# Optimization experiments

Hardware: AMD Instinct MI355X
Metric: run time of the kernel (lower is better)

Reference implementation:

```python
import jax, jax.numpy as jnp
import numpy as np

NEG_INF = -1.0e9
VALID_THRESH = -1.0e8
EPS = 1e-12


def _l2_normalize(x):
    n = jnp.linalg.norm(x, axis=-1, keepdims=True)
    return x / jnp.maximum(n, EPS)


def setup_inputs() -> dict:
    key = jax.random.key(0)
    k1, k2, k3, k4 = jax.random.split(key, 4)
    B, Nq, Nd, D = 64, 32, 256, 128
    return {
        "query_embeds": jax.random.normal(k1, (B, Nq, D), dtype=jnp.float32),
        "query_mask": jax.random.randint(k2, (B, Nq), 0, 2, dtype=jnp.int32),
        "doc_embeds": jax.random.normal(k3, (B, Nd, D), dtype=jnp.float32),
        "doc_mask": jax.random.randint(k4, (B, Nd), 0, 2, dtype=jnp.int32),
    }


def reference(query_embeds, query_mask, doc_embeds, doc_mask):
    # normalize=True, symmetric=True path
    q = _l2_normalize(query_embeds)
    d = _l2_normalize(doc_embeds)
    qm = query_mask.astype(jnp.float32)[..., None]  # [B, Nq, 1]
    dm = doc_mask.astype(jnp.float32)[..., None]    # [B, Nd, 1]
    q = q * qm
    d = d * dm

    # token_sims: [Bq, Bd, Nq, Nd]
    token_sims = jnp.einsum("qtd,csd->qcts", q, d)
    # pair mask: [Bq,1,Nq,1] * [1,Bd,1,Nd]
    mask = qm[:, None, :, :] * dm[None, :, :, 0][:, :, None, :].transpose(1, 0, 2, 3)
    masked_sims = jnp.where(mask > 0, token_sims, NEG_INF)

    # query -> doc max over doc tokens
    q2d = jnp.max(masked_sims, axis=-1)          # [Bq, Bd, Nq]
    valid_q = (q2d > VALID_THRESH).astype(jnp.float32)
    q2d = jnp.where(valid_q > 0, q2d, 0.0)
    cnt_q = jnp.maximum(jnp.sum(valid_q, axis=-1), 1.0)
    q2d_score = jnp.sum(q2d, axis=-1) / cnt_q    # [Bq, Bd]

    # doc -> query max over query tokens
    d2q = jnp.max(masked_sims, axis=-2)          # [Bq, Bd, Nd]
    valid_d = (d2q > VALID_THRESH).astype(jnp.float32)
    d2q = jnp.where(valid_d > 0, d2q, 0.0)
    cnt_d = jnp.maximum(jnp.sum(valid_d, axis=-1), 1.0)
    d2q_score = jnp.sum(d2q, axis=-1) / cnt_d    # [Bq, Bd]

    return (q2d_score + d2q_score) / 2.0
```

## Files before the change

### kernel.cpp

```cpp
#include <hip/hip_runtime.h>
#include <hip/hip_bf16.h>

typedef short bf16x8 __attribute__((ext_vector_type(8)));
typedef float f32x4 __attribute__((ext_vector_type(4)));

#define B_   64
#define NQ   32
#define ND   256
#define DIM  128
#define NEG_INF_F (-1.0e9f)
#define VALID_F   (-1.0e8f)

__global__ __launch_bounds__(256) void normalize_rows(
    const float* __restrict__ q, const int* __restrict__ qmask,
    const float* __restrict__ d, const int* __restrict__ dmask,
    __hip_bfloat16* __restrict__ qn, __hip_bfloat16* __restrict__ dn)
{
    const int l   = threadIdx.x & 63;
    const int row = blockIdx.x * 4 + (threadIdx.x >> 6);

    const float* src;
    __hip_bfloat16* dst;
    int m;
    if (row < B_ * NQ) {
        src = q + row * DIM;  dst = qn + row * DIM;  m = qmask[row];
    } else {
        const int r2 = row - B_ * NQ;
        src = d + r2 * DIM;   dst = dn + r2 * DIM;   m = dmask[r2];
    }

    const float2 v = *reinterpret_cast<const float2*>(src + l * 2);
    float ss = v.x * v.x + v.y * v.y;
    #pragma unroll
    for (int off = 1; off <= 32; off <<= 1) ss += __shfl_xor(ss, off);

    const float scale = m ? (1.0f / fmaxf(sqrtf(ss), 1e-12f)) : 0.0f;

    __hip_bfloat162 o;
    o.x = __float2bfloat16(v.x * scale);
    o.y = __float2bfloat16(v.y * scale);
    *reinterpret_cast<__hip_bfloat162*>(dst + l * 2) = o;
}

__global__ __launch_bounds__(256) void chamfer_main(
    const __hip_bfloat16* __restrict__ qn,
    const __hip_bfloat16* __restrict__ dn,
    const int* __restrict__ qmask,
    const int* __restrict__ dmask,
    float* __restrict__ out)
{
    const int bq = blockIdx.x >> 6;
    const int bd = blockIdx.x & 63;
    const int tid = threadIdx.x;
    const int w  = tid >> 6;
    const int l  = tid & 63;
    const int lr = l & 15;
    const int lk = l >> 4;

    const __hip_bfloat16* Q  = qn + bq * (NQ * DIM);
    const __hip_bfloat16* Dp = dn + (bd * ND + w * 64) * DIM;

    f32x4 acc[2][4] = {};

    #pragma unroll
    for (int kk = 0; kk < 4; ++kk) {
        const int k0 = kk * 32 + lk * 8;
        const bf16x8 a0 = *reinterpret_cast<const bf16x8*>(Q + lr * DIM + k0);
        const bf16x8 a1 = *reinterpret_cast<const bf16x8*>(Q + (16 + lr) * DIM + k0);
        bf16x8 bfr[4];
        #pragma unroll
        for (int ni = 0; ni < 4; ++ni)
            bfr[ni] = *reinterpret_cast<const bf16x8*>(Dp + (ni * 16 + lr) * DIM + k0);
        #pragma unroll
        for (int ni = 0; ni < 4; ++ni) {
            acc[0][ni] = __builtin_amdgcn_mfma_f32_16x16x32_bf16(a0, bfr[ni], acc[0][ni], 0, 0, 0);
            acc[1][ni] = __builtin_amdgcn_mfma_f32_16x16x32_bf16(a1, bfr[ni], acc[1][ni], 0, 0, 0);
        }
    }

    int qmv[2][4];
    #pragma unroll
    for (int mi = 0; mi < 2; ++mi)
        #pragma unroll
        for (int r = 0; r < 4; ++r)
            qmv[mi][r] = qmask[bq * NQ + mi * 16 + lk * 4 + r];
    int dmv[4];
    #pragma unroll
    for (int ni = 0; ni < 4; ++ni)
        dmv[ni] = dmask[bq * ND + w * 64 + ni * 16 + lr];

    float rmax[2][4];
    float cmax[4];
    #pragma unroll
    for (int ni = 0; ni < 4; ++ni) cmax[ni] = NEG_INF_F;
    #pragma unroll
    for (int mi = 0; mi < 2; ++mi) {
        #pragma unroll
        for (int r = 0; r < 4; ++r) {
            float rm = NEG_INF_F;
            #pragma unroll
            for (int ni = 0; ni < 4; ++ni) {
                const float v = (qmv[mi][r] && dmv[ni]) ? acc[mi][ni][r] : NEG_INF_F;
                rm = fmaxf(rm, v);
                cmax[ni] = fmaxf(cmax[ni], v);
            }
            rmax[mi][r] = rm;
        }
    }

    #pragma unroll
    for (int ni = 0; ni < 4; ++ni) {
        cmax[ni] = fmaxf(cmax[ni], __shfl_xor(cmax[ni], 16));
        cmax[ni] = fmaxf(cmax[ni], __shfl_xor(cmax[ni], 32));
    }
    float sd = 0.0f, cd = 0.0f;
    if (lk == 0) {
        #pragma unroll
        for (int ni = 0; ni < 4; ++ni)
            if (cmax[ni] > VALID_F) { sd += cmax[ni]; cd += 1.0f; }
    }
    #pragma unroll
    for (int off = 1; off <= 32; off <<= 1) {
        sd += __shfl_xor(sd, off);
        cd += __shfl_xor(cd, off);
    }

    __shared__ float s_rmax[4][NQ];
    __shared__ float s_sd[4], s_cd[4];
    if (l == 0) { s_sd[w] = sd; s_cd[w] = cd; }

    #pragma unroll
    for (int mi = 0; mi < 2; ++mi) {
        #pragma unroll
        for (int r = 0; r < 4; ++r) {
            #pragma unroll
            for (int off = 1; off <= 8; off <<= 1)
                rmax[mi][r] = fmaxf(rmax[mi][r], __shfl_xor(rmax[mi][r], off));
        }
    }
    if (lr == 0) {
        #pragma unroll
        for (int mi = 0; mi < 2; ++mi)
            #pragma unroll
            for (int r = 0; r < 4; ++r)
                s_rmax[w][mi * 16 + lk * 4 + r] = rmax[mi][r];
    }
    __syncthreads();

    if (w == 0) {
        float v = NEG_INF_F;
        if (l < NQ) {
            #pragma unroll
            for (int wv = 0; wv < 4; ++wv) v = fmaxf(v, s_rmax[wv][l]);
        }
        float sq = 0.0f, cq = 0.0f;
        if (l < NQ && v > VALID_F) { sq = v; cq = 1.0f; }
        #pragma unroll
        for (int off = 1; off <= 32; off <<= 1) {
            sq += __shfl_xor(sq, off);
            cq += __shfl_xor(cq, off);
        }
        if (l == 0) {
            const float q2d = sq / fmaxf(cq, 1.0f);
            const float sdt = s_sd[0] + s_sd[1] + s_sd[2] + s_sd[3];
            const float cdt = s_cd[0] + s_cd[1] + s_cd[2] + s_cd[3];
            const float d2q = sdt / fmaxf(cdt, 1.0f);
            out[bq * B_ + bd] = 0.5f * (q2d + d2q);
        }
    }
}

extern "C" void kernel_launch(void* const* d_in, const int* in_sizes, int n_in,
                              void* d_out, int out_size, void* d_ws, size_t ws_size,
                              hipStream_t stream) {
    const float* q  = (const float*)d_in[0];
    const int*   qm = (const int*)d_in[1];
    const float* d  = (const float*)d_in[2];
    const int*   dm = (const int*)d_in[3];
    float* out = (float*)d_out;

    __hip_bfloat16* qn = (__hip_bfloat16*)d_ws;
    __hip_bfloat16* dn = qn + (B_ * NQ) * DIM;

    normalize_rows<<<(B_ * NQ + B_ * ND) / 4, 256, 0, stream>>>(q, qm, d, dm, qn, dn);
    chamfer_main<<<B_ * B_, 256, 0, stream>>>(qn, dn, qm, dm, out);
}
```

Measured before the change: 117.2 us.

## Tile four query batches per block to reuse doc fragments, vectorize normalize

Each chamfer block now processes four query batches against one document tile, loading the document bf16 fragments once and reusing them across all four MFMA groups. The grid shrinks by four and each wave finalizes one query batch's score. The normalize kernel is also widened so each thread handles eight elements with 16-byte loads and stores. The exchange is higher accumulator register pressure and less block-level parallelism.

New measurement: 115.5 us. About the same (-1.4%).

```diff
diff --git a/kernel.cpp b/kernel.cpp
--- a/kernel.cpp
+++ b/kernel.cpp
@@ -2,12 +2,14 @@
 #include <hip/hip_bf16.h>
 
 typedef short bf16x8 __attribute__((ext_vector_type(8)));
+typedef short short8 __attribute__((ext_vector_type(8)));
 typedef float f32x4 __attribute__((ext_vector_type(4)));
 
 #define B_   64
 #define NQ   32
 #define ND   256
 #define DIM  128
+#define MT   4
 #define NEG_INF_F (-1.0e9f)
 #define VALID_F   (-1.0e8f)
 
@@ -16,8 +18,9 @@
     const float* __restrict__ d, const int* __restrict__ dmask,
     __hip_bfloat16* __restrict__ qn, __hip_bfloat16* __restrict__ dn)
 {
-    const int l   = threadIdx.x & 63;
-    const int row = blockIdx.x * 4 + (threadIdx.x >> 6);
+    const int tid  = threadIdx.x;
+    const int sub  = tid & 15;
+    const int row  = blockIdx.x * 16 + (tid >> 4);
 
     const float* src;
     __hip_bfloat16* dst;
@@ -29,17 +32,23 @@
         src = d + r2 * DIM;   dst = dn + r2 * DIM;   m = dmask[r2];
     }
 
-    const float2 v = *reinterpret_cast<const float2*>(src + l * 2);
-    float ss = v.x * v.x + v.y * v.y;
-    #pragma unroll
-    for (int off = 1; off <= 32; off <<= 1) ss += __shfl_xor(ss, off);
+    const float4 v0 = *reinterpret_cast<const float4*>(src + sub * 8);
+    const float4 v1 = *reinterpret_cast<const float4*>(src + sub * 8 + 4);
+    float ss = v0.x*v0.x + v0.y*v0.y + v0.z*v0.z + v0.w*v0.w
+             + v1.x*v1.x + v1.y*v1.y + v1.z*v1.z + v1.w*v1.w;
+    #pragma unroll
+    for (int off = 1; off <= 8; off <<= 1) ss += __shfl_xor(ss, off);
 
     const float scale = m ? (1.0f / fmaxf(sqrtf(ss), 1e-12f)) : 0.0f;
 
-    __hip_bfloat162 o;
-    o.x = __float2bfloat16(v.x * scale);
-    o.y = __float2bfloat16(v.y * scale);
-    *reinterpret_cast<__hip_bfloat162*>(dst + l * 2) = o;
+    short8 o;
+    const float f[8] = {v0.x, v0.y, v0.z, v0.w, v1.x, v1.y, v1.z, v1.w};
+    #pragma unroll
+    for (int j = 0; j < 8; ++j) {
+        __hip_bfloat16 b = __float2bfloat16(f[j] * scale);
+        o[j] = *reinterpret_cast<short*>(&b);
+    }
+    *reinterpret_cast<short8*>(dst + sub * 8) = o;
 }
 
 __global__ __launch_bounds__(256) void chamfer_main(
@@ -49,109 +58,117 @@
     const int* __restrict__ dmask,
     float* __restrict__ out)
 {
-    const int bq = blockIdx.x >> 6;
-    const int bd = blockIdx.x & 63;
+    const int bq0 = (blockIdx.x >> 6) * MT;
+    const int bd  = blockIdx.x & 63;
     const int tid = threadIdx.x;
-    const int w  = tid >> 6;
-    const int l  = tid & 63;
-    const int lr = l & 15;
-    const int lk = l >> 4;
-
-    const __hip_bfloat16* Q  = qn + bq * (NQ * DIM);
+    const int w   = tid >> 6;
+    const int l   = tid & 63;
+    const int lr  = l & 15;
+    const int lk  = l >> 4;
+
     const __hip_bfloat16* Dp = dn + (bd * ND + w * 64) * DIM;
 
-    f32x4 acc[2][4] = {};
+    f32x4 acc[MT][2][4] = {};
 
     #pragma unroll
     for (int kk = 0; kk < 4; ++kk) {
         const int k0 = kk * 32 + lk * 8;
-        const bf16x8 a0 = *reinterpret_cast<const bf16x8*>(Q + lr * DIM + k0);
-        const bf16x8 a1 = *reinterpret_cast<const bf16x8*>(Q + (16 + lr) * DIM + k0);
         bf16x8 bfr[4];
         #pragma unroll
         for (int ni = 0; ni < 4; ++ni)
             bfr[ni] = *reinterpret_cast<const bf16x8*>(Dp + (ni * 16 + lr) * DIM + k0);
         #pragma unroll
+        for (int m = 0; m < MT; ++m) {
+            const __hip_bfloat16* Q = qn + (bq0 + m) * (NQ * DIM);
+            const bf16x8 a0 = *reinterpret_cast<const bf16x8*>(Q + lr * DIM + k0);
+            const bf16x8 a1 = *reinterpret_cast<const bf16x8*>(Q + (16 + lr) * DIM + k0);
+            #pragma unroll
+            for (int ni = 0; ni < 4; ++ni) {
+                acc[m][0][ni] = __builtin_amdgcn_mfma_f32_16x16x32_bf16(a0, bfr[ni], acc[m][0][ni], 0, 0, 0);
+                acc[m][1][ni] = __builtin_amdgcn_mfma_f32_16x16x32_bf16(a1, bfr[ni], acc[m][1][ni], 0, 0, 0);
+            }
+        }
+    }
+
+    __shared__ float s_rmax[4][MT][NQ];
+    __shared__ float s_sd[4][MT], s_cd[4][MT];
+
+    #pragma unroll
+    for (int m = 0; m < MT; ++m) {
+        const int bq = bq0 + m;
+        int qmv[2][4];
+        #pragma unroll
+        for (int mi = 0; mi < 2; ++mi)
+            #pragma unroll
+            for (int r = 0; r < 4; ++r)
+                qmv[mi][r] = qmask[bq * NQ + mi * 16 + lk * 4 + r];
+        int dmv[4];
+        #pragma unroll
+        for (int ni = 0; ni < 4; ++ni)
+            dmv[ni] = dmask[bq * ND + w * 64 + ni * 16 + lr];
+
+        float rmax[2][4];
+        float cmax[4];
+        #pragma unroll
+        for (int ni = 0; ni < 4; ++ni) cmax[ni] = NEG_INF_F;
+        #pragma unroll
+        for (int mi = 0; mi < 2; ++mi) {
+            #pragma unroll
+            for (int r = 0; r < 4; ++r) {
+                float rm = NEG_INF_F;
+                #pragma unroll
+                for (int ni = 0; ni < 4; ++ni) {
+                    const float v = (qmv[mi][r] && dmv[ni]) ? acc[m][mi][ni][r] : NEG_INF_F;
+                    rm = fmaxf(rm, v);
+                    cmax[ni] = fmaxf(cmax[ni], v);
+                }
+                rmax[mi][r] = rm;
+            }
+        }
+
+        #pragma unroll
         for (int ni = 0; ni < 4; ++ni) {
-            acc[0][ni] = __builtin_amdgcn_mfma_f32_16x16x32_bf16(a0, bfr[ni], acc[0][ni], 0, 0, 0);
-            acc[1][ni] = __builtin_amdgcn_mfma_f32_16x16x32_bf16(a1, bfr[ni], acc[1][ni], 0, 0, 0);
-        }
-    }
-
-    int qmv[2][4];
-    #pragma unroll
-    for (int mi = 0; mi < 2; ++mi)
-        #pragma unroll
-        for (int r = 0; r < 4; ++r)
-            qmv[mi][r] = qmask[bq * NQ + mi * 16 + lk * 4 + r];
-    int dmv[4];
-    #pragma unroll
-    for (int ni = 0; ni < 4; ++ni)
-        dmv[ni] = dmask[bq * ND + w * 64 + ni * 16 + lr];
-
-    float rmax[2][4];
-    float cmax[4];
-    #pragma unroll
-    for (int ni = 0; ni < 4; ++ni) cmax[ni] = NEG_INF_F;
-    #pragma unroll
-    for (int mi = 0; mi < 2; ++mi) {
-        #pragma unroll
-        for (int r = 0; r < 4; ++r) {
-            float rm = NEG_INF_F;
-            #pragma unroll
-            for (int ni = 0; ni < 4; ++ni) {
-                const float v = (qmv[mi][r] && dmv[ni]) ? acc[mi][ni][r] : NEG_INF_F;
-                rm = fmaxf(rm, v);
-                cmax[ni] = fmaxf(cmax[ni], v);
+            cmax[ni] = fmaxf(cmax[ni], __shfl_xor(cmax[ni], 16));
+            cmax[ni] = fmaxf(cmax[ni], __shfl_xor(cmax[ni], 32));
+        }
+        float sd = 0.0f, cd = 0.0f;
+        if (lk == 0) {
+            #pragma unroll
+            for (int ni = 0; ni < 4; ++ni)
+                if (cmax[ni] > VALID_F) { sd += cmax[ni]; cd += 1.0f; }
+        }
+        #pragma unroll
+        for (int off = 1; off <= 32; off <<= 1) {
+            sd += __shfl_xor(sd, off);
+            cd += __shfl_xor(cd, off);
+        }
+        if (l == 0) { s_sd[w][m] = sd; s_cd[w][m] = cd; }
+
+        #pragma unroll
+        for (int mi = 0; mi < 2; ++mi) {
+            #pragma unroll
+            for (int r = 0; r < 4; ++r) {
+                #pragma unroll
+                for (int off = 1; off <= 8; off <<= 1)
+                    rmax[mi][r] = fmaxf(rmax[mi][r], __shfl_xor(rmax[mi][r], off));
             }
-            rmax[mi][r] = rm;
-        }
-    }
-
-    #pragma unroll
-    for (int ni = 0; ni < 4; ++ni) {
-        cmax[ni] = fmaxf(cmax[ni], __shfl_xor(cmax[ni], 16));
-        cmax[ni] = fmaxf(cmax[ni], __shfl_xor(cmax[ni], 32));
-    }
-    float sd = 0.0f, cd = 0.0f;
-    if (lk == 0) {
-        #pragma unroll
-        for (int ni = 0; ni < 4; ++ni)
-            if (cmax[ni] > VALID_F) { sd += cmax[ni]; cd += 1.0f; }
-    }
-    #pragma unroll
-    for (int off = 1; off <= 32; off <<= 1) {
-        sd += __shfl_xor(sd, off);
-        cd += __shfl_xor(cd, off);
-    }
-
-    __shared__ float s_rmax[4][NQ];
-    __shared__ float s_sd[4], s_cd[4];
-    if (l == 0) { s_sd[w] = sd; s_cd[w] = cd; }
-
-    #pragma unroll
-    for (int mi = 0; mi < 2; ++mi) {
-        #pragma unroll
-        for (int r = 0; r < 4; ++r) {
-            #pragma unroll
-            for (int off = 1; off <= 8; off <<= 1)
-                rmax[mi][r] = fmaxf(rmax[mi][r], __shfl_xor(rmax[mi][r], off));
-        }
-    }
-    if (lr == 0) {
-        #pragma unroll
-        for (int mi = 0; mi < 2; ++mi)
-            #pragma unroll
-            for (int r = 0; r < 4; ++r)
-                s_rmax[w][mi * 16 + lk * 4 + r] = rmax[mi][r];
+        }
+        if (lr == 0) {
+            #pragma unroll
+            for (int mi = 0; mi < 2; ++mi)
+                #pragma unroll
+                for (int r = 0; r < 4; ++r)
+                    s_rmax[w][m][mi * 16 + lk * 4 + r] = rmax[mi][r];
+        }
     }
     __syncthreads();
 
-    if (w == 0) {
+    {
+        const int m = w;
         float v = NEG_INF_F;
         if (l < NQ) {
             #pragma unroll
-            for (int wv = 0; wv < 4; ++wv) v = fmaxf(v, s_rmax[wv][l]);
+            for (int wv = 0; wv < 4; ++wv) v = fmaxf(v, s_rmax[wv][m][l]);
         }
         float sq = 0.0f, cq = 0.0f;
         if (l < NQ && v > VALID_F) { sq = v; cq = 1.0f; }
@@ -162,10 +179,10 @@
         }
         if (l == 0) {
             const float q2d = sq / fmaxf(cq, 1.0f);
-            const float sdt = s_sd[0] + s_sd[1] + s_sd[2] + s_sd[3];
-            const float cdt = s_cd[0] + s_cd[1] + s_cd[2] + s_cd[3];
+            const float sdt = s_sd[0][m] + s_sd[1][m] + s_sd[2][m] + s_sd[3][m];
+            const float cdt = s_cd[0][m] + s_cd[1][m] + s_cd[2][m] + s_cd[3][m];
             const float d2q = sdt / fmaxf(cdt, 1.0f);
-            out[bq * B_ + bd] = 0.5f * (q2d + d2q);
+            out[(bq0 + m) * B_ + bd] = 0.5f * (q2d + d2q);
         }
     }
 }
@@ -182,6 +199,6 @@
     __hip_bfloat16* qn = (__hip_bfloat16*)d_ws;
     __hip_bfloat16* dn = qn + (B_ * NQ) * DIM;
 
-    normalize_rows<<<(B_ * NQ + B_ * ND) / 4, 256, 0, stream>>>(q, qm, d, dm, qn, dn);
-    chamfer_main<<<B_ * B_, 256, 0, stream>>>(qn, dn, qm, dm, out);
+    normalize_rows<<<(B_ * NQ + B_ * ND) / 16, 256, 0, stream>>>(q, qm, d, dm, qn, dn);
+    chamfer_main<<<(B_ / MT) * B_, 256, 0, stream>>>(qn, dn, qm, dm, out);
 }
```
